# Performance work log

Measured on AMD Instinct MI355X. Metric: run time of the kernel, lower is better.

The kernel has to match this reference:

```python
import jax, jax.numpy as jnp
import numpy as np

B, N, D4 = 32768, 20, 64  # embed_dim = 4 * D4 = 256
BIG = 1e10


def setup_inputs() -> dict:
    key = jax.random.key(0)
    ks = jax.random.split(key, 10)
    points = jax.random.normal(ks[0], (B, N, 3), dtype=jnp.float32)
    mask = (jax.random.uniform(ks[1], (B, N)) < 0.85).astype(jnp.float32)
    s = 0.1
    return {
        "points": points,
        "mask": mask,
        "W_rel": jax.random.normal(ks[2], (3, D4), jnp.float32) * s,
        "b_rel": jax.random.normal(ks[3], (D4,), jnp.float32) * s,
        "W_dist": jax.random.normal(ks[4], (1, D4), jnp.float32) * s,
        "b_dist": jax.random.normal(ks[5], (D4,), jnp.float32) * s,
        "emb_count": jax.random.normal(ks[6], (50, D4), jnp.float32) * s,
        "W_den": jax.random.normal(ks[7], (1, D4), jnp.float32) * s,
        "b_den": jax.random.normal(ks[8], (D4,), jnp.float32) * s,
    }


def _local_density(points, mask):
    # Batched replacement of the per-sample cdist+topk Python loop.
    b, n, _ = points.shape
    diff = points[:, :, None, :] - points[:, None, :, :]        # [B,N,N,3]
    d2 = jnp.sum(diff * diff, axis=-1)                          # [B,N,N]
    eye = jnp.eye(n, dtype=bool)
    pair_valid = (mask[:, :, None] > 0) & (mask[:, None, :] > 0) & ~eye
    d = jnp.where(pair_valid, jnp.sqrt(jnp.maximum(d2, 1e-12)), BIG)
    nearest = -jax.lax.top_k(-d, 3)[0]                          # 3 smallest dists, ascending
    nv = jnp.sum(mask, axis=1).astype(jnp.int32)                # [B] valid counts
    k = jnp.clip(jnp.minimum(3, nv - 1), 1, None)               # k = min(3, n_valid-1)
    w = (jnp.arange(3)[None, :] < k[:, None]).astype(points.dtype)  # [B,3]
    dens = jnp.sum(nearest * w[:, None, :], axis=-1) / k[:, None].astype(points.dtype)
    valid_row = (mask > 0) & (nv[:, None] > 1)                  # zero for invalid / n_valid<=1
    return jnp.where(valid_row, dens, 0.0)[..., None]           # [B,N,1]


def reference(points, mask, W_rel, b_rel, W_dist, b_dist, emb_count, W_den, b_den):
    b, n, _ = points.shape
    n_valid = jnp.clip(jnp.sum(mask, axis=1, keepdims=True), 1, None)    # [B,1]
    centroid = jnp.sum(points * mask[..., None], axis=1, keepdims=True) / n_valid[..., None]
    rel = points - centroid                                              # [B,N,3]
    rel_f = rel @ W_rel + b_rel                                          # [B,N,D4]
    cdist_ = jnp.linalg.norm(rel, axis=-1, keepdims=True)                # [B,N,1]
    dist_f = cdist_ @ W_dist + b_dist                                    # [B,N,D4]
    idx = n_valid[:, 0].astype(jnp.int32)                                # [B]
    count_f = jnp.broadcast_to(emb_count[idx][:, None, :], (b, n, emb_count.shape[1]))
    density = _local_density(points, mask)                               # [B,N,1]
    den_f = density @ W_den + b_den                                      # [B,N,D4]
    return jnp.concatenate([rel_f, dist_f, count_f, den_f], axis=-1)     # [B,N,4*D4]
```

## Files before the change

### kernel.cpp

```cpp
#include <hip/hip_runtime.h>
#include <math.h>

#define BIGD 1e10f
#define NPTS 20
#define BPB  4

typedef float f4 __attribute__((ext_vector_type(4)));

__device__ __forceinline__ void wave_lds_fence() {
    asm volatile("s_waitcnt lgkmcnt(0)" ::: "memory");
    __builtin_amdgcn_sched_barrier(0);
}

__global__ __launch_bounds__(256) void spf_kernel(
    const float* __restrict__ points,
    const float* __restrict__ mask,
    const float* __restrict__ W_rel,
    const float* __restrict__ b_rel,
    const float* __restrict__ W_dist,
    const float* __restrict__ b_dist,
    const float* __restrict__ emb_count,
    const float* __restrict__ W_den,
    const float* __restrict__ b_den,
    float* __restrict__ out,
    int B)
{
    const int w    = threadIdx.x >> 6;
    const int lane = threadIdx.x & 63;
    const int b    = blockIdx.x * BPB + w;
    if (b >= B) return;

    __shared__ __align__(16) f4    sPM[BPB][NPTS];
    __shared__ __align__(16) f4    sRC[BPB][NPTS];
    __shared__          float sDen[BPB][NPTS];

    if (lane < NPTS) {
        const float* pp = points + (size_t)b * (NPTS * 3) + lane * 3;
        f4 q;
        q.x = pp[0]; q.y = pp[1]; q.z = pp[2];
        q.w = mask[(size_t)b * NPTS + lane];
        sPM[w][lane] = q;
    }
    wave_lds_fence();

    float sm = 0.f, cx = 0.f, cy = 0.f, cz = 0.f;
#pragma unroll
    for (int i = 0; i < NPTS; ++i) {
        const f4 q = sPM[w][i];
        sm += q.w;
        cx = fmaf(q.w, q.x, cx);
        cy = fmaf(q.w, q.y, cy);
        cz = fmaf(q.w, q.z, cz);
    }
    const float nvf = fmaxf(sm, 1.0f);
    cx /= nvf; cy /= nvf; cz /= nvf;
    const int nv  = (int)(sm + 0.5f);
    const int idx = (int)(nvf + 0.5f);

    if (lane < NPTS) {
        const f4 me = sPM[w][lane];
        const float mi = me.w;
        float b0 = BIGD, b1 = BIGD, b2 = BIGD;
#pragma unroll
        for (int j = 0; j < NPTS; ++j) {
            const f4 qj = sPM[w][j];
            const float dx = me.x - qj.x;
            const float dy = me.y - qj.y;
            const float dz = me.z - qj.z;
            const float d2 = dx * dx + dy * dy + dz * dz;
            float d = sqrtf(fmaxf(d2, 1e-12f));
            const bool valid = (j != lane) && (mi > 0.f) && (qj.w > 0.f);
            d = valid ? d : BIGD;
            if (d < b0)      { b2 = b1; b1 = b0; b0 = d; }
            else if (d < b1) { b2 = b1; b1 = d; }
            else if (d < b2) { b2 = d; }
        }
        int k = min(3, nv - 1);
        k = max(k, 1);
        float s = b0;
        if (k > 1) s += b1;
        if (k > 2) s += b2;
        const float dens = s / (float)k;
        sDen[w][lane] = ((mi > 0.f) && (nv > 1)) ? dens : 0.f;

        f4 rc;
        rc.x = me.x - cx; rc.y = me.y - cy; rc.z = me.z - cz;
        rc.w = sqrtf(rc.x * rc.x + rc.y * rc.y + rc.z * rc.z);
        sRC[w][lane] = rc;
    }
    wave_lds_fence();

    const int region = lane >> 4;
    const int cq     = lane & 15;

    f4 w0 = {0,0,0,0}, w1 = {0,0,0,0}, w2 = {0,0,0,0};
    f4 wd = {0,0,0,0}, bb = {0,0,0,0};
    if (region == 0) {
        w0 = ((const f4*)(W_rel +   0))[cq];
        w1 = ((const f4*)(W_rel +  64))[cq];
        w2 = ((const f4*)(W_rel + 128))[cq];
        bb = ((const f4*)b_rel)[cq];
    } else if (region == 1) {
        wd = ((const f4*)W_dist)[cq];
        bb = ((const f4*)b_dist)[cq];
    } else if (region == 2) {
        bb = ((const f4*)(emb_count + (size_t)idx * 64))[cq];
    } else {
        wd = ((const f4*)W_den)[cq];
        bb = ((const f4*)b_den)[cq];
    }
    const bool use_cd = (region == 1);

    f4* __restrict__ outv = (f4*)(out + (size_t)b * (NPTS * 256));
#pragma unroll
    for (int n = 0; n < NPTS; ++n) {
        const f4 rc = sRC[w][n];
        const float dn = sDen[w][n];
        const float sc = use_cd ? rc.w : dn;
        f4 v;
        v.x = fmaf(rc.x, w0.x, fmaf(rc.y, w1.x, fmaf(rc.z, w2.x, fmaf(sc, wd.x, bb.x))));
        v.y = fmaf(rc.x, w0.y, fmaf(rc.y, w1.y, fmaf(rc.z, w2.y, fmaf(sc, wd.y, bb.y))));
        v.z = fmaf(rc.x, w0.z, fmaf(rc.y, w1.z, fmaf(rc.z, w2.z, fmaf(sc, wd.z, bb.z))));
        v.w = fmaf(rc.x, w0.w, fmaf(rc.y, w1.w, fmaf(rc.z, w2.w, fmaf(sc, wd.w, bb.w))));
        outv[n * 64 + lane] = v;
    }
}

extern "C" void kernel_launch(void* const* d_in, const int* in_sizes, int n_in,
                              void* d_out, int out_size, void* d_ws, size_t ws_size,
                              hipStream_t stream) {
    const float* points    = (const float*)d_in[0];
    const float* mask      = (const float*)d_in[1];
    const float* W_rel     = (const float*)d_in[2];
    const float* b_rel     = (const float*)d_in[3];
    const float* W_dist    = (const float*)d_in[4];
    const float* b_dist    = (const float*)d_in[5];
    const float* emb_count = (const float*)d_in[6];
    const float* W_den     = (const float*)d_in[7];
    const float* b_den     = (const float*)d_in[8];
    float* out             = (float*)d_out;

    const int B    = in_sizes[0] / (NPTS * 3);
    const int grid = (B + BPB - 1) / BPB;
    spf_kernel<<<grid, 256, 0, stream>>>(points, mask, W_rel, b_rel, W_dist, b_dist,
                                         emb_count, W_den, b_den, out, B);
}
```

Measured before the change: 683.8 us.

## Make kernel persistent with grid-stride loop and register prefetch of next batch

Launches a fixed grid of 2048 blocks. Each wave loops over batches with a grid stride, prefetching the next batch's points and mask into registers while computing and storing the current one. Weight and bias loads are hoisted out of the loop, and only the count embedding is fetched per batch. The aim is to hide global load latency and amortize launch and setup costs. The trade-off is fewer resident waves, which may limit the number of outstanding stores.

```diff
diff --git a/kernel.cpp b/kernel.cpp
--- a/kernel.cpp
+++ b/kernel.cpp
@@ -27,72 +27,15 @@
 {
     const int w    = threadIdx.x >> 6;
     const int lane = threadIdx.x & 63;
-    const int b    = blockIdx.x * BPB + w;
-    if (b >= B) return;
+    const int wid  = blockIdx.x * BPB + w;
+    const int nw   = gridDim.x * BPB;
 
     __shared__ __align__(16) f4    sPM[BPB][NPTS];
     __shared__ __align__(16) f4    sRC[BPB][NPTS];
     __shared__          float sDen[BPB][NPTS];
 
-    if (lane < NPTS) {
-        const float* pp = points + (size_t)b * (NPTS * 3) + lane * 3;
-        f4 q;
-        q.x = pp[0]; q.y = pp[1]; q.z = pp[2];
-        q.w = mask[(size_t)b * NPTS + lane];
-        sPM[w][lane] = q;
-    }
-    wave_lds_fence();
-
-    float sm = 0.f, cx = 0.f, cy = 0.f, cz = 0.f;
-#pragma unroll
-    for (int i = 0; i < NPTS; ++i) {
-        const f4 q = sPM[w][i];
-        sm += q.w;
-        cx = fmaf(q.w, q.x, cx);
-        cy = fmaf(q.w, q.y, cy);
-        cz = fmaf(q.w, q.z, cz);
-    }
-    const float nvf = fmaxf(sm, 1.0f);
-    cx /= nvf; cy /= nvf; cz /= nvf;
-    const int nv  = (int)(sm + 0.5f);
-    const int idx = (int)(nvf + 0.5f);
-
-    if (lane < NPTS) {
-        const f4 me = sPM[w][lane];
-        const float mi = me.w;
-        float b0 = BIGD, b1 = BIGD, b2 = BIGD;
-#pragma unroll
-        for (int j = 0; j < NPTS; ++j) {
-            const f4 qj = sPM[w][j];
-            const float dx = me.x - qj.x;
-            const float dy = me.y - qj.y;
-            const float dz = me.z - qj.z;
-            const float d2 = dx * dx + dy * dy + dz * dz;
-            float d = sqrtf(fmaxf(d2, 1e-12f));
-            const bool valid = (j != lane) && (mi > 0.f) && (qj.w > 0.f);
-            d = valid ? d : BIGD;
-            if (d < b0)      { b2 = b1; b1 = b0; b0 = d; }
-            else if (d < b1) { b2 = b1; b1 = d; }
-            else if (d < b2) { b2 = d; }
-        }
-        int k = min(3, nv - 1);
-        k = max(k, 1);
-        float s = b0;
-        if (k > 1) s += b1;
-        if (k > 2) s += b2;
-        const float dens = s / (float)k;
-        sDen[w][lane] = ((mi > 0.f) && (nv > 1)) ? dens : 0.f;
-
-        f4 rc;
-        rc.x = me.x - cx; rc.y = me.y - cy; rc.z = me.z - cz;
-        rc.w = sqrtf(rc.x * rc.x + rc.y * rc.y + rc.z * rc.z);
-        sRC[w][lane] = rc;
-    }
-    wave_lds_fence();
-
     const int region = lane >> 4;
     const int cq     = lane & 15;
-
     f4 w0 = {0,0,0,0}, w1 = {0,0,0,0}, w2 = {0,0,0,0};
     f4 wd = {0,0,0,0}, bb = {0,0,0,0};
     if (region == 0) {
@@ -103,26 +46,97 @@
     } else if (region == 1) {
         wd = ((const f4*)W_dist)[cq];
         bb = ((const f4*)b_dist)[cq];
-    } else if (region == 2) {
-        bb = ((const f4*)(emb_count + (size_t)idx * 64))[cq];
-    } else {
+    } else if (region == 3) {
         wd = ((const f4*)W_den)[cq];
         bb = ((const f4*)b_den)[cq];
     }
     const bool use_cd = (region == 1);
 
-    f4* __restrict__ outv = (f4*)(out + (size_t)b * (NPTS * 256));
+    int b = wid;
+    f4 q = {0,0,0,0};
+    if (b < B && lane < NPTS) {
+        const float* pp = points + (size_t)b * (NPTS * 3) + lane * 3;
+        q.x = pp[0]; q.y = pp[1]; q.z = pp[2];
+        q.w = mask[(size_t)b * NPTS + lane];
+    }
+
+    while (b < B) {
+        const int bn = b + nw;
+
+        if (lane < NPTS) sPM[w][lane] = q;
+        wave_lds_fence();
+
+        if (bn < B && lane < NPTS) {
+            const float* pp = points + (size_t)bn * (NPTS * 3) + lane * 3;
+            q.x = pp[0]; q.y = pp[1]; q.z = pp[2];
+            q.w = mask[(size_t)bn * NPTS + lane];
+        }
+
+        float sm = 0.f, cx = 0.f, cy = 0.f, cz = 0.f;
 #pragma unroll
-    for (int n = 0; n < NPTS; ++n) {
-        const f4 rc = sRC[w][n];
-        const float dn = sDen[w][n];
-        const float sc = use_cd ? rc.w : dn;
-        f4 v;
-        v.x = fmaf(rc.x, w0.x, fmaf(rc.y, w1.x, fmaf(rc.z, w2.x, fmaf(sc, wd.x, bb.x))));
-        v.y = fmaf(rc.x, w0.y, fmaf(rc.y, w1.y, fmaf(rc.z, w2.y, fmaf(sc, wd.y, bb.y))));
-        v.z = fmaf(rc.x, w0.z, fmaf(rc.y, w1.z, fmaf(rc.z, w2.z, fmaf(sc, wd.z, bb.z))));
-        v.w = fmaf(rc.x, w0.w, fmaf(rc.y, w1.w, fmaf(rc.z, w2.w, fmaf(sc, wd.w, bb.w))));
-        outv[n * 64 + lane] = v;
+        for (int i = 0; i < NPTS; ++i) {
+            const f4 p = sPM[w][i];
+            sm += p.w;
+            cx = fmaf(p.w, p.x, cx);
+            cy = fmaf(p.w, p.y, cy);
+            cz = fmaf(p.w, p.z, cz);
+        }
+        const float nvf = fmaxf(sm, 1.0f);
+        cx /= nvf; cy /= nvf; cz /= nvf;
+        const int nv  = (int)(sm + 0.5f);
+        const int idx = (int)(nvf + 0.5f);
+
+        if (lane < NPTS) {
+            const f4 me = sPM[w][lane];
+            const float mi = me.w;
+            float b0 = BIGD, b1 = BIGD, b2 = BIGD;
+#pragma unroll
+            for (int j = 0; j < NPTS; ++j) {
+                const f4 qj = sPM[w][j];
+                const float dx = me.x - qj.x;
+                const float dy = me.y - qj.y;
+                const float dz = me.z - qj.z;
+                const float d2 = dx * dx + dy * dy + dz * dz;
+                float d = sqrtf(fmaxf(d2, 1e-12f));
+                const bool valid = (j != lane) && (mi > 0.f) && (qj.w > 0.f);
+                d = valid ? d : BIGD;
+                if (d < b0)      { b2 = b1; b1 = b0; b0 = d; }
+                else if (d < b1) { b2 = b1; b1 = d; }
+                else if (d < b2) { b2 = d; }
+            }
+            int k = min(3, nv - 1);
+            k = max(k, 1);
+            float s = b0;
+            if (k > 1) s += b1;
+            if (k > 2) s += b2;
+            const float dens = s / (float)k;
+            sDen[w][lane] = ((mi > 0.f) && (nv > 1)) ? dens : 0.f;
+
+            f4 rc;
+            rc.x = me.x - cx; rc.y = me.y - cy; rc.z = me.z - cz;
+            rc.w = sqrtf(rc.x * rc.x + rc.y * rc.y + rc.z * rc.z);
+            sRC[w][lane] = rc;
+        }
+        wave_lds_fence();
+
+        f4 bbi = bb;
+        if (region == 2) bbi = ((const f4*)(emb_count + (size_t)idx * 64))[cq];
+
+        f4* __restrict__ outv = (f4*)(out + (size_t)b * (NPTS * 256));
+#pragma unroll
+        for (int n = 0; n < NPTS; ++n) {
+            const f4 rc = sRC[w][n];
+            const float dn = sDen[w][n];
+            const float sc = use_cd ? rc.w : dn;
+            f4 v;
+            v.x = fmaf(rc.x, w0.x, fmaf(rc.y, w1.x, fmaf(rc.z, w2.x, fmaf(sc, wd.x, bbi.x))));
+            v.y = fmaf(rc.x, w0.y, fmaf(rc.y, w1.y, fmaf(rc.z, w2.y, fmaf(sc, wd.y, bbi.y))));
+            v.z = fmaf(rc.x, w0.z, fmaf(rc.y, w1.z, fmaf(rc.z, w2.z, fmaf(sc, wd.z, bbi.z))));
+            v.w = fmaf(rc.x, w0.w, fmaf(rc.y, w1.w, fmaf(rc.z, w2.w, fmaf(sc, wd.w, bbi.w))));
+            outv[n * 64 + lane] = v;
+        }
+
+        b = bn;
     }
 }
 
@@ -140,8 +154,8 @@
     const float* b_den     = (const float*)d_in[8];
     float* out             = (float*)d_out;
 
-    const int B    = in_sizes[0] / (NPTS * 3);
-    const int grid = (B + BPB - 1) / BPB;
+    const int B = in_sizes[0] / (NPTS * 3);
+    const int grid = 2048;
     spf_kernel<<<grid, 256, 0, stream>>>(points, mask, W_rel, b_rel, W_dist, b_dist,
                                          emb_count, W_den, b_den, out, B);
 }
```

After: 686.5 us. No clear change (+0.4%).
